# Optimization experiments

Measured on AMD Instinct MI355X. Metric: run time of the kernel, lower is better.

The kernel has to match this reference:

```python
import jax, jax.numpy as jnp
import numpy as np

QUANT = 6                      # quant bits
LEVELS = 2 ** QUANT - 1        # quant_levels = 63


def setup_inputs() -> dict:
    key = jax.random.key(0)
    k1, k2, k3 = jax.random.split(key, 3)
    B, C_in, C_out, H, W = 8, 256, 256, 64, 64
    x = jax.random.normal(k1, (B, C_in, H, W), dtype=jnp.float32)
    # 1x1 conv weight stored as [out_channels, in_channels] (kernel dims are 1)
    weight = jax.random.normal(k2, (C_out, C_in), dtype=jnp.float32) * 0.05
    bias = jax.random.normal(k3, (C_out,), dtype=jnp.float32) * 0.05
    return {"x": x, "weight": weight, "bias": bias}


def reference(x, weight, bias):
    """NoiseConv.forward with hard_weight set, mode='batch':
    channel_wise_quantize -> hardware_inference -> float cast.
    (Original computes in float64 on CUDA; here float32 for jit/accel friendliness.)
    """
    # --- channel_wise_quantize (input is detached in torch) ---
    xd = jax.lax.stop_gradient(x)
    cmax = jnp.max(xd, axis=1, keepdims=True)           # [B,1,H,W]
    cmin = jnp.min(xd, axis=1, keepdims=True)           # [B,1,H,W]
    scaling = (cmax - cmin) / LEVELS                    # [B,1,H,W]
    x_int = jnp.round((xd - cmin) / scaling).astype(jnp.int32)  # [B,C,H,W] in [0,63]
    bit_idx = jnp.arange(QUANT, dtype=jnp.int32)
    bits = ((x_int[..., None] >> bit_idx) & 1).astype(x.dtype)   # [B,C,H,W,Q] bitplanes

    # --- hardware_inference (batch mode): one 1x1 conv per bitplane, then
    # weighted recombination with 2^b. Fused here into a single einsum; the
    # math is identical since conv is linear and bitplane values are exact. ---
    base = (2.0 ** jnp.arange(QUANT)).astype(x.dtype)   # quant_base
    out_sum = jnp.einsum('bchwq,q,oc->bohw', bits, base, weight)  # [B,O,H,W]
    out_w = out_sum * scaling                           # per-pixel rescale

    # min-offset term: conv2d(cmin * ones_like(x_plane), weight, bias).
    # cmin is constant across input channels, so it equals cmin * sum_c(w) + bias.
    wsum = jnp.sum(weight, axis=1)                      # [O]
    out_w = out_w + cmin * wsum[None, :, None, None] + bias[None, :, None, None]

    return out_w.astype(jnp.float32)
```

## Files before the change

kernel.cpp:

```cpp
#include <hip/hip_runtime.h>
#include <stdint.h>

#define CI 256
#define CO 256
#define HW 4096
#define PXT 32
#define QP 264

typedef __attribute__((ext_vector_type(8))) short short8;
typedef __attribute__((ext_vector_type(4))) float float4v;

__global__ void prep_kernel(const float* __restrict__ w,
                            ushort* __restrict__ w16,
                            float* __restrict__ wsum) {
    const int o = blockIdx.x;
    const int lane = threadIdx.x;
    float4 v = ((const float4*)(w + o * CI))[lane];
    auto cvt = [](float f) -> ushort {
        uint32_t u = __float_as_uint(f);
        return (ushort)((u + 0x7FFFu + ((u >> 16) & 1u)) >> 16);
    };
    ushort4 q;
    q.x = cvt(v.x); q.y = cvt(v.y); q.z = cvt(v.z); q.w = cvt(v.w);
    ((ushort4*)(w16 + o * CI))[lane] = q;
    float s = v.x + v.y + v.z + v.w;
    for (int off = 32; off >= 1; off >>= 1) s += __shfl_down(s, off);
    if (lane == 0) wsum[o] = s;
}

__global__ __launch_bounds__(256, 4)
void noise_conv_kernel(const float* __restrict__ x,
                       const ushort* __restrict__ w16,
                       const float* __restrict__ wsum,
                       const float* __restrict__ bias,
                       float* __restrict__ out) {
    __shared__ ushort Q[PXT * QP];
    __shared__ float Rmn[4][33], Rmx[4][33];
    __shared__ float cmin_s[PXT], s_s[PXT];

    const int t = threadIdx.x;
    const int blk = blockIdx.x;
    const int img = blk >> 7;
    const int p0 = (blk & 127) * PXT;
    const float* xb = x + (size_t)img * CI * HW + p0;

    const int p = t & 31;
    const int cg = t >> 5;
    const int l = t & 63;
    const int wv = t >> 6;

    float xv[32];
    #pragma unroll
    for (int j = 0; j < 32; ++j)
        xv[j] = xb[(size_t)(cg * 32 + j) * HW + p];

    float mn = xv[0], mx = xv[0];
    #pragma unroll
    for (int j = 1; j < 32; ++j) { mn = fminf(mn, xv[j]); mx = fmaxf(mx, xv[j]); }
    mn = fminf(mn, __shfl_xor(mn, 32));
    mx = fmaxf(mx, __shfl_xor(mx, 32));
    if (l < 32) { Rmn[wv][l] = mn; Rmx[wv][l] = mx; }
    __syncthreads();
    if (t < 32) {
        float m0 = Rmn[0][t], m1 = Rmx[0][t];
        #pragma unroll
        for (int s = 1; s < 4; ++s) {
            m0 = fminf(m0, Rmn[s][t]);
            m1 = fmaxf(m1, Rmx[s][t]);
        }
        cmin_s[t] = m0;
        s_s[t] = (m1 - m0) / 63.0f;
    }
    __syncthreads();

    {
        const float cm = cmin_s[p];
        const float iv = 1.0f / s_s[p];
        ushort* qrow = Q + p * QP + cg * 32;
        #pragma unroll
        for (int c4 = 0; c4 < 4; ++c4) {
            uint32_t pk[4];
            #pragma unroll
            for (int j2 = 0; j2 < 4; ++j2) {
                const float q0 = rintf((xv[c4 * 8 + 2 * j2]     - cm) * iv);
                const float q1 = rintf((xv[c4 * 8 + 2 * j2 + 1] - cm) * iv);
                pk[j2] = (__float_as_uint(q0) >> 16) |
                         (__float_as_uint(q1) & 0xFFFF0000u);
            }
            ((uint4*)qrow)[c4] = make_uint4(pk[0], pk[1], pk[2], pk[3]);
        }
    }

    const int m16 = l & 15;
    const int quad = l >> 4;
    const ushort* wrow = w16 + (size_t)(wv * 64) * CI;
    short8 bfc[4];
    #pragma unroll
    for (int nt = 0; nt < 4; ++nt)
        bfc[nt] = *((const short8*)(
            wrow + (size_t)(nt * 16 + m16) * CI + quad * 8));
    __syncthreads();

    float4v acc[2][4];
    #pragma unroll
    for (int mt = 0; mt < 2; ++mt)
        #pragma unroll
        for (int nt = 0; nt < 4; ++nt) {
            float4v z = {0.0f, 0.0f, 0.0f, 0.0f};
            acc[mt][nt] = z;
        }

    {
        short8 af[2];
        #pragma unroll
        for (int mt = 0; mt < 2; ++mt)
            af[mt] = *((const short8*)(Q + (mt * 16 + m16) * QP + quad * 8));
        #pragma unroll
        for (int nt = 0; nt < 4; ++nt)
            #pragma unroll
            for (int mt = 0; mt < 2; ++mt)
                acc[mt][nt] = __builtin_amdgcn_mfma_f32_16x16x32_bf16(
                    af[mt], bfc[nt], acc[mt][nt], 0, 0, 0);
    }
    #pragma unroll
    for (int ks = 1; ks < 8; ++ks) {
        short8 af[2];
        #pragma unroll
        for (int mt = 0; mt < 2; ++mt)
            af[mt] = *((const short8*)(
                Q + (mt * 16 + m16) * QP + ks * 32 + quad * 8));
        #pragma unroll
        for (int nt = 0; nt < 4; ++nt) {
            const short8 bf = *((const short8*)(
                wrow + (size_t)(nt * 16 + m16) * CI + ks * 32 + quad * 8));
            #pragma unroll
            for (int mt = 0; mt < 2; ++mt)
                acc[mt][nt] = __builtin_amdgcn_mfma_f32_16x16x32_bf16(
                    af[mt], bf, acc[mt][nt], 0, 0, 0);
        }
    }

    float* outp = out + (size_t)img * CO * HW + p0;
    #pragma unroll
    for (int mt = 0; mt < 2; ++mt) {
        const int pb = mt * 16 + quad * 4;
        float sv[4], cv[4];
        #pragma unroll
        for (int r = 0; r < 4; ++r) {
            sv[r] = s_s[pb + r];
            cv[r] = cmin_s[pb + r];
        }
        #pragma unroll
        for (int nt = 0; nt < 4; ++nt) {
            const int ch = wv * 64 + nt * 16 + m16;
            const float ws = wsum[ch];
            const float bs = bias[ch];
            float4 o;
            o.x = acc[mt][nt][0] * sv[0] + cv[0] * ws + bs;
            o.y = acc[mt][nt][1] * sv[1] + cv[1] * ws + bs;
            o.z = acc[mt][nt][2] * sv[2] + cv[2] * ws + bs;
            o.w = acc[mt][nt][3] * sv[3] + cv[3] * ws + bs;
            *((float4*)(outp + (size_t)ch * HW + pb)) = o;
        }
    }
}

extern "C" void kernel_launch(void* const* d_in, const int* in_sizes, int n_in,
                              void* d_out, int out_size, void* d_ws, size_t ws_size,
                              hipStream_t stream) {
    const float* x    = (const float*)d_in[0];
    const float* w    = (const float*)d_in[1];
    const float* bias = (const float*)d_in[2];
    float* out = (float*)d_out;

    ushort* w16 = (ushort*)d_ws;
    float* wsum = (float*)((char*)d_ws + (size_t)CO * CI * sizeof(ushort));

    prep_kernel<<<CO, 64, 0, stream>>>(w, w16, wsum);
    noise_conv_kernel<<<1024, 256, 0, stream>>>(x, w16, wsum, bias, out);
}
```

Before: 102.3 us.

## Process two 32-pixel tiles per block with all input loads issued upfront

Each block now handles 64 pixels as two 32-pixel halves and loads the input for both halves into registers before any compute, giving more memory-level parallelism per thread. The grid is halved to 512 blocks and launch bounds drop to 2 blocks per SM to allow the extra registers. The weight-fragment register cache for the first k-step is removed. The trade-off is fewer resident waves and fewer blocks (512 over 256 CUs), which may reduce latency hiding and load balance.

```diff
diff --git a/kernel.cpp b/kernel.cpp
--- a/kernel.cpp
+++ b/kernel.cpp
@@ -28,7 +28,7 @@
     if (lane == 0) wsum[o] = s;
 }
 
-__global__ __launch_bounds__(256, 4)
+__global__ __launch_bounds__(256, 2)
 void noise_conv_kernel(const float* __restrict__ x,
                        const ushort* __restrict__ w16,
                        const float* __restrict__ wsum,
@@ -40,128 +40,120 @@
 
     const int t = threadIdx.x;
     const int blk = blockIdx.x;
-    const int img = blk >> 7;
-    const int p0 = (blk & 127) * PXT;
-    const float* xb = x + (size_t)img * CI * HW + p0;
+    const int img = blk >> 6;
+    const int p0b = (blk & 63) * 64;
+    const float* xb = x + (size_t)img * CI * HW;
+    float* outb = out + (size_t)img * CO * HW;
 
     const int p = t & 31;
     const int cg = t >> 5;
     const int l = t & 63;
     const int wv = t >> 6;
-
-    float xv[32];
-    #pragma unroll
-    for (int j = 0; j < 32; ++j)
-        xv[j] = xb[(size_t)(cg * 32 + j) * HW + p];
-
-    float mn = xv[0], mx = xv[0];
-    #pragma unroll
-    for (int j = 1; j < 32; ++j) { mn = fminf(mn, xv[j]); mx = fmaxf(mx, xv[j]); }
-    mn = fminf(mn, __shfl_xor(mn, 32));
-    mx = fmaxf(mx, __shfl_xor(mx, 32));
-    if (l < 32) { Rmn[wv][l] = mn; Rmx[wv][l] = mx; }
-    __syncthreads();
-    if (t < 32) {
-        float m0 = Rmn[0][t], m1 = Rmx[0][t];
-        #pragma unroll
-        for (int s = 1; s < 4; ++s) {
-            m0 = fminf(m0, Rmn[s][t]);
-            m1 = fmaxf(m1, Rmx[s][t]);
-        }
-        cmin_s[t] = m0;
-        s_s[t] = (m1 - m0) / 63.0f;
-    }
-    __syncthreads();
-
-    {
-        const float cm = cmin_s[p];
-        const float iv = 1.0f / s_s[p];
-        ushort* qrow = Q + p * QP + cg * 32;
-        #pragma unroll
-        for (int c4 = 0; c4 < 4; ++c4) {
-            uint32_t pk[4];
-            #pragma unroll
-            for (int j2 = 0; j2 < 4; ++j2) {
-                const float q0 = rintf((xv[c4 * 8 + 2 * j2]     - cm) * iv);
-                const float q1 = rintf((xv[c4 * 8 + 2 * j2 + 1] - cm) * iv);
-                pk[j2] = (__float_as_uint(q0) >> 16) |
-                         (__float_as_uint(q1) & 0xFFFF0000u);
-            }
-            ((uint4*)qrow)[c4] = make_uint4(pk[0], pk[1], pk[2], pk[3]);
-        }
-    }
-
     const int m16 = l & 15;
     const int quad = l >> 4;
-    const ushort* wrow = w16 + (size_t)(wv * 64) * CI;
-    short8 bfc[4];
+
+    float xv[2][32];
     #pragma unroll
-    for (int nt = 0; nt < 4; ++nt)
-        bfc[nt] = *((const short8*)(
-            wrow + (size_t)(nt * 16 + m16) * CI + quad * 8));
-    __syncthreads();
+    for (int h = 0; h < 2; ++h)
+        #pragma unroll
+        for (int j = 0; j < 32; ++j)
+            xv[h][j] = xb[(size_t)(cg * 32 + j) * HW + p0b + h * 32 + p];
 
-    float4v acc[2][4];
     #pragma unroll
-    for (int mt = 0; mt < 2; ++mt)
+    for (int h = 0; h < 2; ++h) {
+        const int p0 = p0b + h * 32;
+
+        float mn = xv[h][0], mx = xv[h][0];
         #pragma unroll
-        for (int nt = 0; nt < 4; ++nt) {
-            float4v z = {0.0f, 0.0f, 0.0f, 0.0f};
-            acc[mt][nt] = z;
+        for (int j = 1; j < 32; ++j) {
+            mn = fminf(mn, xv[h][j]);
+            mx = fmaxf(mx, xv[h][j]);
+        }
+        mn = fminf(mn, __shfl_xor(mn, 32));
+        mx = fmaxf(mx, __shfl_xor(mx, 32));
+        if (l < 32) { Rmn[wv][l] = mn; Rmx[wv][l] = mx; }
+        __syncthreads();
+        if (t < 32) {
+            float m0 = Rmn[0][t], m1 = Rmx[0][t];
+            #pragma unroll
+            for (int s = 1; s < 4; ++s) {
+                m0 = fminf(m0, Rmn[s][t]);
+                m1 = fmaxf(m1, Rmx[s][t]);
+            }
+            cmin_s[t] = m0;
+            s_s[t] = (m1 - m0) / 63.0f;
+        }
+        __syncthreads();
+
+        {
+            const float cm = cmin_s[p];
+            const float iv = 1.0f / s_s[p];
+            ushort* qrow = Q + p * QP + cg * 32;
+            #pragma unroll
+            for (int c4 = 0; c4 < 4; ++c4) {
+                uint32_t pk[4];
+                #pragma unroll
+                for (int j2 = 0; j2 < 4; ++j2) {
+                    const float q0 = rintf((xv[h][c4 * 8 + 2 * j2]     - cm) * iv);
+                    const float q1 = rintf((xv[h][c4 * 8 + 2 * j2 + 1] - cm) * iv);
+                    pk[j2] = (__float_as_uint(q0) >> 16) |
+                             (__float_as_uint(q1) & 0xFFFF0000u);
+                }
+                ((uint4*)qrow)[c4] = make_uint4(pk[0], pk[1], pk[2], pk[3]);
+            }
+        }
+        __syncthreads();
+
+        float4v acc[2][4];
+        #pragma unroll
+        for (int mt = 0; mt < 2; ++mt)
+            #pragma unroll
+            for (int nt = 0; nt < 4; ++nt) {
+                float4v z = {0.0f, 0.0f, 0.0f, 0.0f};
+                acc[mt][nt] = z;
+            }
+        const ushort* wrow = w16 + (size_t)(wv * 64) * CI;
+        #pragma unroll
+        for (int ks = 0; ks < 8; ++ks) {
+            short8 af[2];
+            #pragma unroll
+            for (int mt = 0; mt < 2; ++mt)
+                af[mt] = *((const short8*)(
+                    Q + (mt * 16 + m16) * QP + ks * 32 + quad * 8));
+            #pragma unroll
+            for (int nt = 0; nt < 4; ++nt) {
+                const short8 bf = *((const short8*)(
+                    wrow + (size_t)(nt * 16 + m16) * CI + ks * 32 + quad * 8));
+                #pragma unroll
+                for (int mt = 0; mt < 2; ++mt)
+                    acc[mt][nt] = __builtin_amdgcn_mfma_f32_16x16x32_bf16(
+                        af[mt], bf, acc[mt][nt], 0, 0, 0);
+            }
         }
 
-    {
-        short8 af[2];
         #pragma unroll
-        for (int mt = 0; mt < 2; ++mt)
-            af[mt] = *((const short8*)(Q + (mt * 16 + m16) * QP + quad * 8));
-        #pragma unroll
-        for (int nt = 0; nt < 4; ++nt)
+        for (int mt = 0; mt < 2; ++mt) {
+            const int pb = mt * 16 + quad * 4;
+            float sv[4], cv[4];
             #pragma unroll
-            for (int mt = 0; mt < 2; ++mt)
-                acc[mt][nt] = __builtin_amdgcn_mfma_f32_16x16x32_bf16(
-                    af[mt], bfc[nt], acc[mt][nt], 0, 0, 0);
-    }
-    #pragma unroll
-    for (int ks = 1; ks < 8; ++ks) {
-        short8 af[2];
-        #pragma unroll
-        for (int mt = 0; mt < 2; ++mt)
-            af[mt] = *((const short8*)(
-                Q + (mt * 16 + m16) * QP + ks * 32 + quad * 8));
-        #pragma unroll
-        for (int nt = 0; nt < 4; ++nt) {
-            const short8 bf = *((const short8*)(
-                wrow + (size_t)(nt * 16 + m16) * CI + ks * 32 + quad * 8));
+            for (int r = 0; r < 4; ++r) {
+                sv[r] = s_s[pb + r];
+                cv[r] = cmin_s[pb + r];
+            }
             #pragma unroll
-            for (int mt = 0; mt < 2; ++mt)
-                acc[mt][nt] = __builtin_amdgcn_mfma_f32_16x16x32_bf16(
-                    af[mt], bf, acc[mt][nt], 0, 0, 0);
+            for (int nt = 0; nt < 4; ++nt) {
+                const int ch = wv * 64 + nt * 16 + m16;
+                const float ws = wsum[ch];
+                const float bs = bias[ch];
+                float4 o;
+                o.x = acc[mt][nt][0] * sv[0] + cv[0] * ws + bs;
+                o.y = acc[mt][nt][1] * sv[1] + cv[1] * ws + bs;
+                o.z = acc[mt][nt][2] * sv[2] + cv[2] * ws + bs;
+                o.w = acc[mt][nt][3] * sv[3] + cv[3] * ws + bs;
+                *((float4*)(outb + (size_t)ch * HW + p0 + pb)) = o;
+            }
         }
-    }
-
-    float* outp = out + (size_t)img * CO * HW + p0;
-    #pragma unroll
-    for (int mt = 0; mt < 2; ++mt) {
-        const int pb = mt * 16 + quad * 4;
-        float sv[4], cv[4];
-        #pragma unroll
-        for (int r = 0; r < 4; ++r) {
-            sv[r] = s_s[pb + r];
-            cv[r] = cmin_s[pb + r];
-        }
-        #pragma unroll
-        for (int nt = 0; nt < 4; ++nt) {
-            const int ch = wv * 64 + nt * 16 + m16;
-            const float ws = wsum[ch];
-            const float bs = bias[ch];
-            float4 o;
-            o.x = acc[mt][nt][0] * sv[0] + cv[0] * ws + bs;
-            o.y = acc[mt][nt][1] * sv[1] + cv[1] * ws + bs;
-            o.z = acc[mt][nt][2] * sv[2] + cv[2] * ws + bs;
-            o.w = acc[mt][nt][3] * sv[3] + cv[3] * ws + bs;
-            *((float4*)(outp + (size_t)ch * HW + pb)) = o;
-        }
+        if (h == 0) __syncthreads();
     }
 }
 
@@ -177,5 +169,5 @@
     float* wsum = (float*)((char*)d_ws + (size_t)CO * CI * sizeof(ushort));
 
     prep_kernel<<<CO, 64, 0, stream>>>(w, w16, wsum);
-    noise_conv_kernel<<<1024, 256, 0, stream>>>(x, w16, wsum, bias, out);
+    noise_conv_kernel<<<512, 256, 0, stream>>>(x, w16, wsum, bias, out);
 }
```

New measurement: 101.6 us. About the same (-0.6%).
